# Kernel tuning notes

Hardware: AMD Instinct MI355X
Metric: run time of the kernel (lower is better)

The kernel has to match this reference:

```python
import jax, jax.numpy as jnp
import numpy as np

EPS = 1e-6


def setup_inputs() -> dict:
    key = jax.random.key(0)
    k1, k2, k3 = jax.random.split(key, 3)
    N, E, CIN, COUT = 50000, 800000, 128, 128
    x = jax.random.normal(k1, (N, CIN), dtype=jnp.float32)
    edge_index = jax.random.randint(k2, (2, E), 0, N, dtype=jnp.int64)
    # Xavier-uniform weight as in reset_parameters
    limit = float(np.sqrt(6.0 / (CIN + COUT)))
    weight = jax.random.uniform(k3, (CIN, COUT), minval=-limit, maxval=limit, dtype=jnp.float32)
    bias = jnp.zeros((COUT,), dtype=jnp.float32)
    return {"x": x, "edge_index": edge_index, "weight": weight, "bias": bias}


def reference(x, edge_index, weight, bias):
    # x: [N, Cin], edge_index: [2, E]
    N = x.shape[0]
    src, dst = edge_index[0], edge_index[1]
    ones = jnp.ones(src.shape, dtype=x.dtype)
    # degree counts (== torch.bincount with minlength=N)
    src_deg = jax.ops.segment_sum(ones, src, num_segments=N)  # [N]
    dst_deg = jax.ops.segment_sum(ones, dst, num_segments=N)  # [N]
    src_inv = jax.lax.rsqrt(src_deg + EPS)
    dst_inv = jax.lax.rsqrt(dst_deg + EPS)
    edge_norm = src_inv[src] * dst_inv[dst]  # [E]
    msg = x[src] * edge_norm[:, None]  # [E, Cin] normalized source features
    # Equivalent to the dense one-hot einsum('ef,en->nf'): segment-sum over dst
    aggregated = jax.ops.segment_sum(msg, dst, num_segments=N)  # [N, Cin]
    # add_self_loops=False branch
    return aggregated @ weight + bias
```

## Files before the change

### kernel.cpp

```cpp
#include <hip/hip_runtime.h>
#include <math.h>

#define EPS 1e-6f
#define CAP 64

__device__ inline unsigned short f2bf(float f) {
    unsigned u = __float_as_uint(f);
    unsigned r = u + 0x7FFFu + ((u >> 16) & 1u);
    return (unsigned short)(r >> 16);
}

__global__ __launch_bounds__(256, 2)
void k_fused(const int* __restrict__ ei, int E,
             int* __restrict__ deg_src, int* __restrict__ deg_dst,
             int* __restrict__ slots,
             const float* __restrict__ x, const float* __restrict__ w,
             unsigned short* __restrict__ y, int N, int G) {
    __shared__ float4 wlds[128 * 32];
    int b = (int)blockIdx.x;
    bool isGemm;
    int  idx;
    if (b < 2 * G) { isGemm = ((b & 1) == 0); idx = b >> 1; }
    else           { isGemm = false;          idx = b - G;  }

    if (!isGemm) {
        int e = idx * 256 + (int)threadIdx.x;
        if (e < E) {
            int s = ei[e];
            int d = ei[E + e];
            atomicAdd(&deg_src[s], 1);
            int r = atomicAdd(&deg_dst[d], 1);
            if (r < CAP) slots[(size_t)d * CAP + r] = s;
        }
        return;
    }

    int t = threadIdx.x;
    const float4* w4 = (const float4*)w;
    #pragma unroll
    for (int i = 0; i < 16; ++i)
        wlds[t + 256 * i] = w4[t + 256 * i];
    __syncthreads();

    int tx = t & 31;
    int ty = t >> 5;
    int rowBase = idx * 64 + ty * 8;

    float4 acc[8];
    #pragma unroll
    for (int r = 0; r < 8; ++r) acc[r] = make_float4(0.f, 0.f, 0.f, 0.f);

    const float4* x4 = (const float4*)x;

    if (rowBase + 8 <= N) {
        #pragma unroll 1
        for (int k4 = 0; k4 < 32; ++k4) {
            float4 xv[8];
            #pragma unroll
            for (int r = 0; r < 8; ++r)
                xv[r] = x4[(size_t)(rowBase + r) * 32 + k4];
            #pragma unroll
            for (int kk = 0; kk < 4; ++kk) {
                float4 wv = wlds[(k4 * 4 + kk) * 32 + tx];
                #pragma unroll
                for (int r = 0; r < 8; ++r) {
                    float xs = (kk == 0) ? xv[r].x : (kk == 1) ? xv[r].y
                             : (kk == 2) ? xv[r].z : xv[r].w;
                    acc[r].x += xs * wv.x;
                    acc[r].y += xs * wv.y;
                    acc[r].z += xs * wv.z;
                    acc[r].w += xs * wv.w;
                }
            }
        }
        #pragma unroll
        for (int r = 0; r < 8; ++r) {
            ushort4 us;
            us.x = f2bf(acc[r].x); us.y = f2bf(acc[r].y);
            us.z = f2bf(acc[r].z); us.w = f2bf(acc[r].w);
            ((ushort4*)(y + (size_t)(rowBase + r) * 128))[tx] = us;
        }
    } else {
        #pragma unroll 1
        for (int k4 = 0; k4 < 32; ++k4) {
            float4 xv[8];
            #pragma unroll
            for (int r = 0; r < 8; ++r)
                xv[r] = (rowBase + r < N) ? x4[(size_t)(rowBase + r) * 32 + k4]
                                          : make_float4(0.f, 0.f, 0.f, 0.f);
            #pragma unroll
            for (int kk = 0; kk < 4; ++kk) {
                float4 wv = wlds[(k4 * 4 + kk) * 32 + tx];
                #pragma unroll
                for (int r = 0; r < 8; ++r) {
                    float xs = (kk == 0) ? xv[r].x : (kk == 1) ? xv[r].y
                             : (kk == 2) ? xv[r].z : xv[r].w;
                    acc[r].x += xs * wv.x;
                    acc[r].y += xs * wv.y;
                    acc[r].z += xs * wv.z;
                    acc[r].w += xs * wv.w;
                }
            }
        }
        #pragma unroll
        for (int r = 0; r < 8; ++r) {
            if (rowBase + r < N) {
                ushort4 us;
                us.x = f2bf(acc[r].x); us.y = f2bf(acc[r].y);
                us.z = f2bf(acc[r].z); us.w = f2bf(acc[r].w);
                ((ushort4*)(y + (size_t)(rowBase + r) * 128))[tx] = us;
            }
        }
    }
}

__launch_bounds__(256)
__global__ void k_gather(const int* __restrict__ deg_src, const int* __restrict__ deg_dst,
                         const int* __restrict__ slots,
                         const unsigned* __restrict__ y1,
                         const float* __restrict__ bias,
                         float* __restrict__ out, int N) {
    int gid  = blockIdx.x * blockDim.x + threadIdx.x;
    int node = gid >> 6;
    int lane = gid & 63;
    if (node >= N) return;
    int dd  = deg_dst[node];
    int end = dd < CAP ? dd : CAP;
    const int* list = slots + (size_t)node * CAP;

    float ax0 = 0.f, ay0 = 0.f, ax1 = 0.f, ay1 = 0.f;
    float ax2 = 0.f, ay2 = 0.f, ax3 = 0.f, ay3 = 0.f;

    int j = 0;
    #pragma unroll 1
    for (; j + 16 <= end; j += 16) {
        int s[16]; unsigned v[16]; float c[16];
        #pragma unroll
        for (int u = 0; u < 16; ++u) s[u] = list[j + u];
        #pragma unroll
        for (int u = 0; u < 16; ++u) v[u] = y1[(size_t)s[u] * 64 + lane];
        #pragma unroll
        for (int u = 0; u < 16; ++u) c[u] = rsqrtf((float)deg_src[s[u]] + EPS);
        #pragma unroll
        for (int u = 0; u < 16; u += 4) {
            ax0 += c[u+0] * __uint_as_float(v[u+0] << 16); ay0 += c[u+0] * __uint_as_float(v[u+0] & 0xffff0000u);
            ax1 += c[u+1] * __uint_as_float(v[u+1] << 16); ay1 += c[u+1] * __uint_as_float(v[u+1] & 0xffff0000u);
            ax2 += c[u+2] * __uint_as_float(v[u+2] << 16); ay2 += c[u+2] * __uint_as_float(v[u+2] & 0xffff0000u);
            ax3 += c[u+3] * __uint_as_float(v[u+3] << 16); ay3 += c[u+3] * __uint_as_float(v[u+3] & 0xffff0000u);
        }
    }
    if (j + 8 <= end) {
        int s[8]; unsigned v[8]; float c[8];
        #pragma unroll
        for (int u = 0; u < 8; ++u) s[u] = list[j + u];
        #pragma unroll
        for (int u = 0; u < 8; ++u) v[u] = y1[(size_t)s[u] * 64 + lane];
        #pragma unroll
        for (int u = 0; u < 8; ++u) c[u] = rsqrtf((float)deg_src[s[u]] + EPS);
        #pragma unroll
        for (int u = 0; u < 8; u += 4) {
            ax0 += c[u+0] * __uint_as_float(v[u+0] << 16); ay0 += c[u+0] * __uint_as_float(v[u+0] & 0xffff0000u);
            ax1 += c[u+1] * __uint_as_float(v[u+1] << 16); ay1 += c[u+1] * __uint_as_float(v[u+1] & 0xffff0000u);
            ax2 += c[u+2] * __uint_as_float(v[u+2] << 16); ay2 += c[u+2] * __uint_as_float(v[u+2] & 0xffff0000u);
            ax3 += c[u+3] * __uint_as_float(v[u+3] << 16); ay3 += c[u+3] * __uint_as_float(v[u+3] & 0xffff0000u);
        }
        j += 8;
    }
    if (j + 4 <= end) {
        int s0 = list[j + 0], s1 = list[j + 1];
        int s2 = list[j + 2], s3 = list[j + 3];
        unsigned v0 = y1[(size_t)s0 * 64 + lane];
        unsigned v1 = y1[(size_t)s1 * 64 + lane];
        unsigned v2 = y1[(size_t)s2 * 64 + lane];
        unsigned v3 = y1[(size_t)s3 * 64 + lane];
        float c0 = rsqrtf((float)deg_src[s0] + EPS);
        float c1 = rsqrtf((float)deg_src[s1] + EPS);
        float c2 = rsqrtf((float)deg_src[s2] + EPS);
        float c3 = rsqrtf((float)deg_src[s3] + EPS);
        ax0 += c0 * __uint_as_float(v0 << 16); ay0 += c0 * __uint_as_float(v0 & 0xffff0000u);
        ax1 += c1 * __uint_as_float(v1 << 16); ay1 += c1 * __uint_as_float(v1 & 0xffff0000u);
        ax2 += c2 * __uint_as_float(v2 << 16); ay2 += c2 * __uint_as_float(v2 & 0xffff0000u);
        ax3 += c3 * __uint_as_float(v3 << 16); ay3 += c3 * __uint_as_float(v3 & 0xffff0000u);
        j += 4;
    }
    #pragma unroll 1
    for (; j < end; ++j) {
        int s = list[j];
        unsigned v = y1[(size_t)s * 64 + lane];
        float c = rsqrtf((float)deg_src[s] + EPS);
        ax0 += c * __uint_as_float(v << 16); ay0 += c * __uint_as_float(v & 0xffff0000u);
    }

    float nd = rsqrtf((float)dd + EPS);
    float accx = ((ax0 + ax1) + (ax2 + ax3)) * nd;
    float accy = ((ay0 + ay1) + (ay2 + ay3)) * nd;
    float2 b = ((const float2*)bias)[lane];
    ((float2*)out)[(size_t)node * 64 + lane] = make_float2(accx + b.x, accy + b.y);
}

extern "C" void kernel_launch(void* const* d_in, const int* in_sizes, int n_in,
                              void* d_out, int out_size, void* d_ws, size_t ws_size,
                              hipStream_t stream) {
    const float* x    = (const float*)d_in[0];
    const int*   ei   = (const int*)d_in[1];
    const float* w    = (const float*)d_in[2];
    const float* bias = (const float*)d_in[3];
    float*       out  = (float*)d_out;

    const int C = 128;
    const int N = in_sizes[0] / C;
    const int E = in_sizes[1] / 2;

    char* ws = (char*)d_ws;
    size_t off = 0;
    auto alloc = [&](size_t bytes) -> void* {
        void* p = ws + off;
        off += (bytes + 255) & ~(size_t)255;
        return p;
    };
    int*            degblk = (int*)alloc((size_t)2 * N * 4);
    int*            slots  = (int*)alloc((size_t)N * CAP * 4);
    unsigned short* y      = (unsigned short*)alloc((size_t)N * C * 2);
    (void)ws_size;
    int* deg_src = degblk;
    int* deg_dst = degblk + N;

    const int TB = 256;
    hipMemsetAsync(degblk, 0, (size_t)2 * N * 4, stream);

    int degBlocks  = (E + TB - 1) / TB;
    int gemmBlocks = (N + 63) / 64;
    k_fused<<<degBlocks + gemmBlocks, TB, 0, stream>>>(
        ei, E, deg_src, deg_dst, slots, x, w, y, N, gemmBlocks);

    long long gthreads = (long long)N * 64;
    k_gather<<<(int)((gthreads + TB - 1) / TB), TB, 0, stream>>>(
        deg_src, deg_dst, slots, (const unsigned*)y, bias, out, N);
}
```

Baseline: 204.8 us.

## Compute source degrees with LDS histogram blocks instead of global atomics

Adds 32 dedicated blocks at the front of the fused launch. Each one scans all source indices and builds a shared-memory histogram for its own range of nodes, then writes the counts to deg_src. The per-edge global atomicAdd on deg_src is removed from the edge blocks. Each histogram block reads the whole source-index array (800k ints), so these 32 blocks can become a long tail that extends the kernel's critical path, in exchange for fewer contended global atomics.

```diff
diff --git a/kernel.cpp b/kernel.cpp
--- a/kernel.cpp
+++ b/kernel.cpp
@@ -3,6 +3,7 @@
 
 #define EPS 1e-6f
 #define CAP 64
+#define HB  32
 
 __device__ inline unsigned short f2bf(float f) {
     unsigned u = __float_as_uint(f);
@@ -18,24 +19,53 @@
              unsigned short* __restrict__ y, int N, int G) {
     __shared__ float4 wlds[128 * 32];
     int b = (int)blockIdx.x;
+    int t = (int)threadIdx.x;
+
+    if (b < HB) {
+        int binsPerRange = (N + HB - 1) / HB;
+        int base = b * binsPerRange;
+        int hi = N - base; if (hi > binsPerRange) hi = binsPerRange;
+        if (hi <= 0) return;
+        int* bins = (int*)wlds;
+        for (int i = t; i < binsPerRange; i += 256) bins[i] = 0;
+        __syncthreads();
+        const int4* e4 = (const int4*)ei;
+        int nq = E >> 2;
+        #pragma unroll 2
+        for (int i = t; i < nq; i += 256) {
+            int4 v = e4[i];
+            int a;
+            a = v.x - base; if ((unsigned)a < (unsigned)hi) atomicAdd(&bins[a], 1);
+            a = v.y - base; if ((unsigned)a < (unsigned)hi) atomicAdd(&bins[a], 1);
+            a = v.z - base; if ((unsigned)a < (unsigned)hi) atomicAdd(&bins[a], 1);
+            a = v.w - base; if ((unsigned)a < (unsigned)hi) atomicAdd(&bins[a], 1);
+        }
+        for (int i = (nq << 2) + t; i < E; i += 256) {
+            int a = ei[i] - base;
+            if ((unsigned)a < (unsigned)hi) atomicAdd(&bins[a], 1);
+        }
+        __syncthreads();
+        for (int i = t; i < hi; i += 256) deg_src[base + i] = bins[i];
+        return;
+    }
+
+    int b2 = b - HB;
     bool isGemm;
     int  idx;
-    if (b < 2 * G) { isGemm = ((b & 1) == 0); idx = b >> 1; }
-    else           { isGemm = false;          idx = b - G;  }
+    if (b2 < 2 * G) { isGemm = ((b2 & 1) == 0); idx = b2 >> 1; }
+    else            { isGemm = false;           idx = b2 - G;  }
 
     if (!isGemm) {
-        int e = idx * 256 + (int)threadIdx.x;
+        int e = idx * 256 + t;
         if (e < E) {
             int s = ei[e];
             int d = ei[E + e];
-            atomicAdd(&deg_src[s], 1);
             int r = atomicAdd(&deg_dst[d], 1);
             if (r < CAP) slots[(size_t)d * CAP + r] = s;
         }
         return;
     }
 
-    int t = threadIdx.x;
     const float4* w4 = (const float4*)w;
     #pragma unroll
     for (int i = 0; i < 16; ++i)
@@ -230,7 +260,7 @@
 
     int degBlocks  = (E + TB - 1) / TB;
     int gemmBlocks = (N + 63) / 64;
-    k_fused<<<degBlocks + gemmBlocks, TB, 0, stream>>>(
+    k_fused<<<HB + degBlocks + gemmBlocks, TB, 0, stream>>>(
         ei, E, deg_src, deg_dst, slots, x, w, y, N, gemmBlocks);
 
     long long gthreads = (long long)N * 64;
```

Result: slower. 396.1 us (+93.4%).
